# Kernel tuning notes

Hardware: AMD Instinct MI355X
Metric: run time of the kernel (lower is better)

The kernel has to match this reference:

```python
import math
import jax, jax.numpy as jnp
import numpy as np

TAU = 2.0
THR = 1.0
ALPHA = 10.0

T, B, IN_DIM, OUT_DIM = 64, 128, 2048, 2048


def setup_inputs() -> dict:
    key = jax.random.key(0)
    k1, k2, k3 = jax.random.split(key, 3)
    x_seq = jax.random.normal(k1, (T, B, IN_DIM), dtype=jnp.float32)
    # scale like nn.Linear default init so membrane potentials are O(1)
    W = jax.random.normal(k2, (OUT_DIM, IN_DIM), dtype=jnp.float32) / math.sqrt(IN_DIM)
    b = jax.random.normal(k3, (OUT_DIM,), dtype=jnp.float32) * 0.01
    return {"x_seq": x_seq, "W": W, "b": b}


def spike(x):
    # forward: hard threshold (surrogate gradient only matters in bwd)
    return (x > 0).astype(x.dtype)


def reference(x_seq, W, b):
    decay = math.exp(-1.0 / TAU)
    # hoist the linear layer out of the recurrence: one big GEMM
    cur_seq = jnp.einsum("tbi,oi->tbo", x_seq, W) + b  # (T, B, OUT_DIM)
    mem0 = jnp.zeros((x_seq.shape[1], W.shape[0]), dtype=x_seq.dtype)

    def step(mem, cur):
        mem = mem * decay + cur
        spk = spike(mem - THR)
        mem = mem - spk * THR
        return mem, spk

    _, spk_seq = jax.lax.scan(step, mem0, cur_seq)
    return spk_seq  # (T, B, OUT_DIM)
```

## Files before the change

### kernel.cpp

```cpp
#include <hip/hip_runtime.h>
#include <hip/hip_bf16.h>
#include <math.h>


typedef unsigned short u16;
typedef __attribute__((ext_vector_type(8))) short bf16x8;
typedef __attribute__((ext_vector_type(4))) float f32x4;

constexpr int T_STEPS = 64;
constexpr int BATCH   = 128;
constexpr int K_DIM   = 2048;
constexpr int N_DIM   = 2048;
constexpr int M_DIM   = T_STEPS * BATCH;
constexpr int NCHAIN  = BATCH * N_DIM;

constexpr float DECAY_F32 = (float)0.6065306597126334;
constexpr float BAND      = 5e-4f;

#define GLDS16(g, l) __builtin_amdgcn_global_load_lds(                       \
    (const __attribute__((address_space(1))) void*)(g),                      \
    (__attribute__((address_space(3))) void*)(l), 16, 0, 0)

__global__ void zero_counters(unsigned int* p) {
    if (threadIdx.x < 128) p[threadIdx.x] = 0u;
}

__global__ __launch_bounds__(256)
void split_bf16(const float* __restrict__ X, const float* __restrict__ W,
                u16* __restrict__ Ah, u16* __restrict__ Al,
                u16* __restrict__ Wh, u16* __restrict__ Wl) {
    constexpr int NA4 = (M_DIM * K_DIM) / 4;
    constexpr int NW4 = (N_DIM * K_DIM) / 4;
    const int i = blockIdx.x * 256 + threadIdx.x;
    const float* src; u16* dh; u16* dl; int base;
    if (i < NA4)            { src = X; dh = Ah; dl = Al; base = i; }
    else if (i < NA4 + NW4) { src = W; dh = Wh; dl = Wl; base = i - NA4; }
    else return;

    const float4 v = *(const float4*)(src + (size_t)base * 4);
    const float f[4] = {v.x, v.y, v.z, v.w};
    unsigned int hp[2], lp[2];
#pragma unroll
    for (int q = 0; q < 4; q += 2) {
        u16 hh[2], ll[2];
#pragma unroll
        for (int e = 0; e < 2; e++) {
            __hip_bfloat16 hb = __float2bfloat16(f[q + e]);
            const float hf = __bfloat162float(hb);
            __hip_bfloat16 lb = __float2bfloat16(f[q + e] - hf);
            hh[e] = *(u16*)&hb;
            ll[e] = *(u16*)&lb;
        }
        hp[q >> 1] = (unsigned int)hh[0] | ((unsigned int)hh[1] << 16);
        lp[q >> 1] = (unsigned int)ll[0] | ((unsigned int)ll[1] << 16);
    }
    *(uint2*)(dh + (size_t)base * 4) = make_uint2(hp[0], hp[1]);
    *(uint2*)(dl + (size_t)base * 4) = make_uint2(lp[0], lp[1]);
}

__global__ __launch_bounds__(512, 2)
void gemm_bf16x3p(const u16* __restrict__ Ah, const u16* __restrict__ Al,
                  const u16* __restrict__ Bh, const u16* __restrict__ Bl,
                  const float* __restrict__ bias, float* __restrict__ C) {
    extern __shared__ __align__(16) u16 smem[];
    u16* const sAh = smem;
    u16* const sAl = smem + 3 * 8192;
    u16* const sBh = smem + 6 * 8192;
    u16* const sBl = smem + 6 * 8192 + 3 * 4096;

    const int tid  = threadIdx.x;
    const int m0   = blockIdx.y * 256;
    const int n0   = blockIdx.x * 128;
    const int lane = tid & 63;
    const int wave = tid >> 6;
    const int wm   = wave >> 1;
    const int wn   = wave & 1;

    const int cA0 = tid, cA1 = tid + 512, cB0 = tid;
#define OFFA(c) ((size_t)(m0 + ((c) >> 6) * 16 + ((c) & 15)) * K_DIM + (((c) >> 4) & 3) * 8)
#define OFFB(c) ((size_t)(n0 + ((c) >> 6) * 16 + ((c) & 15)) * K_DIM + (((c) >> 4) & 3) * 8)
    const size_t a0 = OFFA(cA0), a1 = OFFA(cA1), b0 = OFFB(cB0);
#undef OFFA
#undef OFFB

    const int lA0 = wave * 512;
    const int lA1 = 4096 + wave * 512;
    const int lB0 = wave * 512;

    f32x4 acc[4][4];
#pragma unroll
    for (int i = 0; i < 4; i++)
#pragma unroll
        for (int j = 0; j < 4; j++) acc[i][j] = (f32x4){0.f, 0.f, 0.f, 0.f};

#define STAGE(s, kc) do {                                                    \
        const int kn_ = (kc) * 32;                                           \
        GLDS16(Ah + a0 + kn_, sAh + (s) * 8192 + lA0);                       \
        GLDS16(Ah + a1 + kn_, sAh + (s) * 8192 + lA1);                       \
        GLDS16(Al + a0 + kn_, sAl + (s) * 8192 + lA0);                       \
        GLDS16(Al + a1 + kn_, sAl + (s) * 8192 + lA1);                       \
        GLDS16(Bh + b0 + kn_, sBh + (s) * 4096 + lB0);                       \
        GLDS16(Bl + b0 + kn_, sBl + (s) * 4096 + lB0);                       \
    } while (0)

#define COMPUTE(rs) do {                                                     \
        bf16x8 fah[4], fal[4], fbh[4], fbl[4];                               \
        _Pragma("unroll")                                                    \
        for (int ti = 0; ti < 4; ti++) {                                     \
            const int ta = wm * 4 + ti;                                      \
            fah[ti] = *(const bf16x8*)&sAh[(rs) * 8192 + (ta * 64 + lane) * 8]; \
            fal[ti] = *(const bf16x8*)&sAl[(rs) * 8192 + (ta * 64 + lane) * 8]; \
        }                                                                    \
        _Pragma("unroll")                                                    \
        for (int tj = 0; tj < 4; tj++) {                                     \
            const int tb = wn * 4 + tj;                                      \
            fbh[tj] = *(const bf16x8*)&sBh[(rs) * 4096 + (tb * 64 + lane) * 8]; \
            fbl[tj] = *(const bf16x8*)&sBl[(rs) * 4096 + (tb * 64 + lane) * 8]; \
        }                                                                    \
        __builtin_amdgcn_s_setprio(1);                                       \
        _Pragma("unroll")                                                    \
        for (int ti = 0; ti < 4; ti++)                                       \
        _Pragma("unroll")                                                    \
        for (int tj = 0; tj < 4; tj++) {                                     \
            acc[ti][tj] = __builtin_amdgcn_mfma_f32_16x16x32_bf16(           \
                fah[ti], fbh[tj], acc[ti][tj], 0, 0, 0);                     \
            acc[ti][tj] = __builtin_amdgcn_mfma_f32_16x16x32_bf16(           \
                fah[ti], fbl[tj], acc[ti][tj], 0, 0, 0);                     \
            acc[ti][tj] = __builtin_amdgcn_mfma_f32_16x16x32_bf16(           \
                fal[ti], fbh[tj], acc[ti][tj], 0, 0, 0);                     \
        }                                                                    \
        __builtin_amdgcn_s_setprio(0);                                       \
    } while (0)

#define SYNC(vm) do {                                                        \
        asm volatile("s_waitcnt vmcnt(" #vm ")" ::: "memory");               \
        __builtin_amdgcn_sched_barrier(0);                                   \
        __builtin_amdgcn_s_barrier();                                        \
        __builtin_amdgcn_sched_barrier(0);                                   \
    } while (0)

    STAGE(0, 0);
    STAGE(1, 1);

    for (int kcb = 0; kcb < 63; kcb += 3) {
        SYNC(6);
        STAGE(2, kcb + 2);
        COMPUTE(0);
        SYNC(6);
        STAGE(0, kcb + 3);
        COMPUTE(1);
        SYNC(6);
        if (kcb + 4 < 64) STAGE(1, kcb + 4);
        COMPUTE(2);
    }
    SYNC(0);
    COMPUTE(0);

#undef SYNC
#undef COMPUTE
#undef STAGE

#pragma unroll
    for (int tj = 0; tj < 4; tj++) {
        const int n  = n0 + wn * 64 + tj * 16 + (lane & 15);
        const float bv = bias[n];
#pragma unroll
        for (int ti = 0; ti < 4; ti++) {
            const int mbase = m0 + wm * 64 + ti * 16 + (lane >> 4) * 4;
#pragma unroll
            for (int r = 0; r < 4; r++)
                C[(size_t)(mbase + r) * N_DIM + n] = acc[ti][tj][r] + bv;
        }
    }
}

__global__ __launch_bounds__(256)
void lif_scan_band(float* __restrict__ buf, unsigned int* __restrict__ counters,
                   unsigned int* __restrict__ worklist) {
    const int idx = blockIdx.x * 256 + threadIdx.x;
    float mem = 0.0f;
    bool flag = false;
#pragma unroll
    for (int t = 0; t < T_STEPS; t++) {
        const size_t off = (size_t)t * NCHAIN + idx;
        mem = __fadd_rn(__fmul_rn(mem, DECAY_F32), buf[off]);
        const float d = __fsub_rn(mem, 1.0f);
        const bool spk = d > 0.0f;
        if (fabsf(d) < BAND) flag = true;
        buf[off] = spk ? 1.0f : 0.0f;
        if (spk) mem = __fsub_rn(mem, 1.0f);
    }
    if (flag) {
        const int b = idx >> 11, o = idx & 2047;
        const unsigned int p = atomicAdd(&counters[b], 1u);
        worklist[b * 2048 + p] = (unsigned int)o;
    }
}

#define RG 16
#define RJ 4
#define BKR 64

__global__ __launch_bounds__(256)
void lif_repair2(const float* __restrict__ X, const float* __restrict__ W,
                 const float* __restrict__ bias,
                 const unsigned int* __restrict__ counters,
                 const unsigned int* __restrict__ worklist,
                 float* __restrict__ out) {
    __shared__ float sX[BKR][T_STEPS + 1];
    __shared__ float sW[RG][BKR + 1];
    __shared__ float scur[T_STEPS][RG + 1];
    __shared__ float sspk[T_STEPS][RG + 1];
    __shared__ int   so[RG];

    const int b = blockIdx.x / RJ;
    const int j = blockIdx.x % RJ;
    const unsigned int n_b = counters[b];
    if (n_b == 0) return;
    const int ngroups = (int)(n_b + RG - 1) / RG;

    const int tid = threadIdx.x;
    const int t   = tid & 63;
    const int oi  = tid >> 6;

    for (int g = j; g < ngroups; g += RJ) {
        if (tid < RG) {
            const int slot = g * RG + tid;
            so[tid] = (slot < (int)n_b) ? (int)worklist[b * 2048 + slot] : -1;
        }
        __syncthreads();

        float Csum[4] = {0.f, 0.f, 0.f, 0.f};
        float P[4]    = {0.f, 0.f, 0.f, 0.f};

        for (int c = 0; c < K_DIM / BKR; c++) {
            if (c > 0 && (c % 5) == 0) {
#pragma unroll
                for (int q = 0; q < 4; q++) {
                    Csum[q] = __fadd_rn(Csum[q], P[q]);
                    P[q] = 0.f;
                }
            }
            const int k0 = c * BKR;
            {
                const int ts = tid & 63;
                const int kq = (tid >> 6) * 16;
                const float* src = &X[(size_t)(ts * BATCH + b) * K_DIM + k0 + kq];
#pragma unroll
                for (int q = 0; q < 4; q++) {
                    const float4 v = *(const float4*)(src + q * 4);
                    sX[kq + q * 4 + 0][ts] = v.x;
                    sX[kq + q * 4 + 1][ts] = v.y;
                    sX[kq + q * 4 + 2][ts] = v.z;
                    sX[kq + q * 4 + 3][ts] = v.w;
                }
            }
            {
                const int wo  = tid >> 4;
                const int wkq = (tid & 15) * 4;
                const int o   = so[wo];
                float4 v = {0.f, 0.f, 0.f, 0.f};
                if (o >= 0) v = *(const float4*)&W[(size_t)o * K_DIM + k0 + wkq];
                sW[wo][wkq + 0] = v.x; sW[wo][wkq + 1] = v.y;
                sW[wo][wkq + 2] = v.z; sW[wo][wkq + 3] = v.w;
            }
            __syncthreads();
#pragma unroll 8
            for (int k = 0; k < BKR; k++) {
                const float xv = sX[k][t];
#pragma unroll
                for (int q = 0; q < 4; q++)
                    P[q] = fmaf(xv, sW[oi * 4 + q][k], P[q]);
            }
            __syncthreads();
        }
#pragma unroll
        for (int q = 0; q < 4; q++) {
            Csum[q] = __fadd_rn(Csum[q], P[q]);
            const int o = so[oi * 4 + q];
            scur[t][oi * 4 + q] = (o >= 0) ? __fadd_rn(Csum[q], bias[o]) : 0.f;
        }
        __syncthreads();
        if (tid < RG && so[tid] >= 0) {
            float mem = 0.0f;
            for (int tt = 0; tt < T_STEPS; tt++) {
                mem = __fadd_rn(__fmul_rn(mem, DECAY_F32), scur[tt][tid]);
                const float d = __fsub_rn(mem, 1.0f);
                const bool spk = d > 0.0f;
                sspk[tt][tid] = spk ? 1.0f : 0.0f;
                if (spk) mem = __fsub_rn(mem, 1.0f);
            }
        }
        __syncthreads();
#pragma unroll
        for (int q = 0; q < 4; q++) {
            const int o = so[oi * 4 + q];
            if (o >= 0)
                out[(size_t)t * NCHAIN + (size_t)b * N_DIM + o] = sspk[t][oi * 4 + q];
        }
        __syncthreads();
    }
}

__global__ __launch_bounds__(256)
void lif_openblas_q320(const float* __restrict__ X, const float* __restrict__ W,
                       const float* __restrict__ bias, float* __restrict__ out) {
    __shared__ float As[16][T_STEPS + 4];
    __shared__ float Ws[16][64 + 4];
    __shared__ float curbuf[T_STEPS][64 + 1];
    const int tid = threadIdx.x;
    const int o0 = blockIdx.x * 64, b0 = blockIdx.y;
    const int tm = (tid & 15) * 4, tn = (tid >> 4) * 4;
    float Csum[4][4], Pacc[4][4];
#pragma unroll
    for (int i = 0; i < 4; i++)
#pragma unroll
        for (int j = 0; j < 4; j++) { Csum[i][j] = 0.f; Pacc[i][j] = 0.f; }
    for (int c = 0; c < K_DIM / 16; c++) {
        if (c > 0 && (c % 20) == 0) {
#pragma unroll
            for (int i = 0; i < 4; i++)
#pragma unroll
                for (int j = 0; j < 4; j++) {
                    Csum[i][j] = __fadd_rn(Csum[i][j], Pacc[i][j]);
                    Pacc[i][j] = 0.f;
                }
        }
        const int k0 = c * 16;
        {
            const int t = tid >> 2, kq = (tid & 3) * 4;
            const float4 av = *(const float4*)&X[(size_t)(t * BATCH + b0) * K_DIM + k0 + kq];
            As[kq + 0][t] = av.x; As[kq + 1][t] = av.y;
            As[kq + 2][t] = av.z; As[kq + 3][t] = av.w;
            const float4 wv = *(const float4*)&W[(size_t)(o0 + t) * K_DIM + k0 + kq];
            Ws[kq + 0][t] = wv.x; Ws[kq + 1][t] = wv.y;
            Ws[kq + 2][t] = wv.z; Ws[kq + 3][t] = wv.w;
        }
        __syncthreads();
#pragma unroll
        for (int k = 0; k < 16; k++) {
            float a[4], w[4];
#pragma unroll
            for (int i = 0; i < 4; i++) a[i] = As[k][tm + i];
#pragma unroll
            for (int j = 0; j < 4; j++) w[j] = Ws[k][tn + j];
#pragma unroll
            for (int i = 0; i < 4; i++)
#pragma unroll
                for (int j = 0; j < 4; j++) Pacc[i][j] = fmaf(a[i], w[j], Pacc[i][j]);
        }
        __syncthreads();
    }
#pragma unroll
    for (int i = 0; i < 4; i++)
#pragma unroll
        for (int j = 0; j < 4; j++)
            curbuf[tm + i][tn + j] =
                __fadd_rn(__fadd_rn(Csum[i][j], Pacc[i][j]), bias[o0 + tn + j]);
    __syncthreads();
    if (tid < 64) {
        float mem = 0.0f;
#pragma unroll
        for (int t = 0; t < T_STEPS; t++) {
            mem = __fadd_rn(__fmul_rn(mem, DECAY_F32), curbuf[t][tid]);
            const float d = __fsub_rn(mem, 1.0f);
            const bool spk = d > 0.0f;
            out[(size_t)t * NCHAIN + (size_t)b0 * N_DIM + o0 + tid] = spk ? 1.0f : 0.0f;
            if (spk) mem = __fsub_rn(mem, 1.0f);
        }
    }
}

extern "C" void kernel_launch(void* const* d_in, const int* in_sizes, int n_in,
                              void* d_out, int out_size, void* d_ws, size_t ws_size,
                              hipStream_t stream) {
    const float* x = nullptr; const float* W = nullptr; const float* bias = nullptr;
    for (int i = 0; i < n_in; i++) {
        if      (in_sizes[i] == M_DIM * K_DIM) x    = (const float*)d_in[i];
        else if (in_sizes[i] == N_DIM * K_DIM) W    = (const float*)d_in[i];
        else if (in_sizes[i] == N_DIM)         bias = (const float*)d_in[i];
    }
    if (!x)    x    = (const float*)d_in[0];
    if (!W)    W    = (const float*)d_in[1];
    if (!bias) bias = (const float*)d_in[2];
    float* out = (float*)d_out;

    const size_t off_cnt = 0;
    const size_t off_wl  = 512;
    const size_t off_Ah  = off_wl + (size_t)128 * 2048 * 4;
    const size_t szA     = (size_t)M_DIM * K_DIM * 2;
    const size_t szW     = (size_t)N_DIM * K_DIM * 2;
    const size_t off_Al  = off_Ah + szA;
    const size_t off_Wh  = off_Al + szA;
    const size_t off_Wl  = off_Wh + szW;
    const size_t need    = off_Wl + szW;

    if (ws_size < need) {
        dim3 grid(N_DIM / 64, BATCH);
        lif_openblas_q320<<<grid, 256, 0, stream>>>(x, W, bias, out);
        return;
    }

    char* ws = (char*)d_ws;
    unsigned int* counters = (unsigned int*)(ws + off_cnt);
    unsigned int* worklist = (unsigned int*)(ws + off_wl);
    u16* Ah = (u16*)(ws + off_Ah);
    u16* Al = (u16*)(ws + off_Al);
    u16* Wh = (u16*)(ws + off_Wh);
    u16* Wl = (u16*)(ws + off_Wl);

    zero_counters<<<1, 128, 0, stream>>>(counters);
    split_bf16<<<(M_DIM * K_DIM / 4 + N_DIM * K_DIM / 4) / 256, 256, 0, stream>>>(
        x, W, Ah, Al, Wh, Wl);
    dim3 ggrid(N_DIM / 128, M_DIM / 256);
    gemm_bf16x3p<<<ggrid, 512, 147456, stream>>>(Ah, Al, Wh, Wl, bias, out);
    lif_scan_band<<<NCHAIN / 256, 256, 0, stream>>>(out, counters, worklist);
    lif_repair2<<<128 * RJ, 256, 0, stream>>>(x, W, bias, counters, worklist, out);
}
```

Before: 481.6 us.

## Double-buffer GEMM register fragments and fold counter zeroing into split kernel

The GEMM main loop now keeps two register fragment sets, loading the next K-chunk from LDS while MFMAs run on the current one. It also prefetches three LDS stages up front and rotates stage indices, with the wait extended to include lgkmcnt. The counter-zeroing launch is merged into the split kernel, removing one kernel launch, and the repair kernel's X tile load is remapped so consecutive threads read contiguous K segments for better coalescing. The extra fragment registers raise VGPR pressure, which may hurt occupancy at 512 threads with 2 blocks per CU.

Result: no change. 472.2 us (-1.9%).

```diff
diff --git a/kernel.cpp b/kernel.cpp
--- a/kernel.cpp
+++ b/kernel.cpp
@@ -21,14 +21,13 @@
     (const __attribute__((address_space(1))) void*)(g),                      \
     (__attribute__((address_space(3))) void*)(l), 16, 0, 0)
 
-__global__ void zero_counters(unsigned int* p) {
-    if (threadIdx.x < 128) p[threadIdx.x] = 0u;
-}
-
 __global__ __launch_bounds__(256)
 void split_bf16(const float* __restrict__ X, const float* __restrict__ W,
                 u16* __restrict__ Ah, u16* __restrict__ Al,
-                u16* __restrict__ Wh, u16* __restrict__ Wl) {
+                u16* __restrict__ Wh, u16* __restrict__ Wl,
+                unsigned int* __restrict__ counters) {
+    if (blockIdx.x == 0 && threadIdx.x < 128) counters[threadIdx.x] = 0u;
+
     constexpr int NA4 = (M_DIM * K_DIM) / 4;
     constexpr int NW4 = (N_DIM * K_DIM) / 4;
     const int i = blockIdx.x * 256 + threadIdx.x;
@@ -59,7 +58,7 @@
 }
 
 __global__ __launch_bounds__(512, 2)
-void gemm_bf16x3p(const u16* __restrict__ Ah, const u16* __restrict__ Al,
+void gemm_bf16x3q(const u16* __restrict__ Ah, const u16* __restrict__ Al,
                   const u16* __restrict__ Bh, const u16* __restrict__ Bl,
                   const float* __restrict__ bias, float* __restrict__ C) {
     extern __shared__ __align__(16) u16 smem[];
@@ -93,47 +92,54 @@
 #pragma unroll
         for (int j = 0; j < 4; j++) acc[i][j] = (f32x4){0.f, 0.f, 0.f, 0.f};
 
+    bf16x8 fahA[4], falA[4], fbhA[4], fblA[4];
+    bf16x8 fahB[4], falB[4], fbhB[4], fblB[4];
+
 #define STAGE(s, kc) do {                                                    \
         const int kn_ = (kc) * 32;                                           \
-        GLDS16(Ah + a0 + kn_, sAh + (s) * 8192 + lA0);                       \
-        GLDS16(Ah + a1 + kn_, sAh + (s) * 8192 + lA1);                       \
-        GLDS16(Al + a0 + kn_, sAl + (s) * 8192 + lA0);                       \
-        GLDS16(Al + a1 + kn_, sAl + (s) * 8192 + lA1);                       \
-        GLDS16(Bh + b0 + kn_, sBh + (s) * 4096 + lB0);                       \
-        GLDS16(Bl + b0 + kn_, sBl + (s) * 4096 + lB0);                       \
+        const int sA_ = (s) * 8192, sB_ = (s) * 4096;                        \
+        GLDS16(Ah + a0 + kn_, sAh + sA_ + lA0);                              \
+        GLDS16(Ah + a1 + kn_, sAh + sA_ + lA1);                              \
+        GLDS16(Al + a0 + kn_, sAl + sA_ + lA0);                              \
+        GLDS16(Al + a1 + kn_, sAl + sA_ + lA1);                              \
+        GLDS16(Bh + b0 + kn_, sBh + sB_ + lB0);                              \
+        GLDS16(Bl + b0 + kn_, sBl + sB_ + lB0);                              \
     } while (0)
 
-#define COMPUTE(rs) do {                                                     \
-        bf16x8 fah[4], fal[4], fbh[4], fbl[4];                               \
+#define LOADF(SET, s) do {                                                   \
+        const int sA_ = (s) * 8192, sB_ = (s) * 4096;                        \
         _Pragma("unroll")                                                    \
         for (int ti = 0; ti < 4; ti++) {                                     \
             const int ta = wm * 4 + ti;                                      \
-            fah[ti] = *(const bf16x8*)&sAh[(rs) * 8192 + (ta * 64 + lane) * 8]; \
-            fal[ti] = *(const bf16x8*)&sAl[(rs) * 8192 + (ta * 64 + lane) * 8]; \
+            fah##SET[ti] = *(const bf16x8*)&sAh[sA_ + (ta * 64 + lane) * 8]; \
+            fal##SET[ti] = *(const bf16x8*)&sAl[sA_ + (ta * 64 + lane) * 8]; \
         }                                                                    \
         _Pragma("unroll")                                                    \
         for (int tj = 0; tj < 4; tj++) {                                     \
             const int tb = wn * 4 + tj;                                      \
-            fbh[tj] = *(const bf16x8*)&sBh[(rs) * 4096 + (tb * 64 + lane) * 8]; \
-            fbl[tj] = *(const bf16x8*)&sBl[(rs) * 4096 + (tb * 64 + lane) * 8]; \
+            fbh##SET[tj] = *(const bf16x8*)&sBh[sB_ + (tb * 64 + lane) * 8]; \
+            fbl##SET[tj] = *(const bf16x8*)&sBl[sB_ + (tb * 64 + lane) * 8]; \
         }                                                                    \
+    } while (0)
+
+#define COMPUTE(SET) do {                                                    \
         __builtin_amdgcn_s_setprio(1);                                       \
         _Pragma("unroll")                                                    \
         for (int ti = 0; ti < 4; ti++)                                       \
         _Pragma("unroll")                                                    \
         for (int tj = 0; tj < 4; tj++) {                                     \
             acc[ti][tj] = __builtin_amdgcn_mfma_f32_16x16x32_bf16(           \
-                fah[ti], fbh[tj], acc[ti][tj], 0, 0, 0);                     \
+                fah##SET[ti], fbh##SET[tj], acc[ti][tj], 0, 0, 0);           \
             acc[ti][tj] = __builtin_amdgcn_mfma_f32_16x16x32_bf16(           \
-                fah[ti], fbl[tj], acc[ti][tj], 0, 0, 0);                     \
+                fah##SET[ti], fbl##SET[tj], acc[ti][tj], 0, 0, 0);           \
             acc[ti][tj] = __builtin_amdgcn_mfma_f32_16x16x32_bf16(           \
-                fal[ti], fbh[tj], acc[ti][tj], 0, 0, 0);                     \
+                fal##SET[ti], fbh##SET[tj], acc[ti][tj], 0, 0, 0);           \
         }                                                                    \
         __builtin_amdgcn_s_setprio(0);                                       \
     } while (0)
 
-#define SYNC(vm) do {                                                        \
-        asm volatile("s_waitcnt vmcnt(" #vm ")" ::: "memory");               \
+#define WAITSYNC(vm) do {                                                    \
+        asm volatile("s_waitcnt vmcnt(" #vm ") lgkmcnt(0)" ::: "memory");    \
         __builtin_amdgcn_sched_barrier(0);                                   \
         __builtin_amdgcn_s_barrier();                                        \
         __builtin_amdgcn_sched_barrier(0);                                   \
@@ -141,23 +147,33 @@
 
     STAGE(0, 0);
     STAGE(1, 1);
-
-    for (int kcb = 0; kcb < 63; kcb += 3) {
-        SYNC(6);
-        STAGE(2, kcb + 2);
-        COMPUTE(0);
-        SYNC(6);
-        STAGE(0, kcb + 3);
-        COMPUTE(1);
-        SYNC(6);
-        if (kcb + 4 < 64) STAGE(1, kcb + 4);
-        COMPUTE(2);
-    }
-    SYNC(0);
-    COMPUTE(0);
-
-#undef SYNC
+    STAGE(2, 2);
+    WAITSYNC(12);
+    LOADF(A, 0);
+
+    int s1 = 1, sW = 0;
+    for (int kc = 0; kc < 62; kc += 2) {
+        WAITSYNC(6);
+        LOADF(B, s1);
+        if (kc + 3 < 64) STAGE(sW, kc + 3);
+        COMPUTE(A);
+        s1 = (s1 == 2) ? 0 : s1 + 1;
+        sW = (sW == 2) ? 0 : sW + 1;
+        WAITSYNC(6);
+        LOADF(A, s1);
+        if (kc + 4 < 64) STAGE(sW, kc + 4);
+        COMPUTE(B);
+        s1 = (s1 == 2) ? 0 : s1 + 1;
+        sW = (sW == 2) ? 0 : sW + 1;
+    }
+    WAITSYNC(0);
+    LOADF(B, s1);
+    COMPUTE(A);
+    COMPUTE(B);
+
+#undef WAITSYNC
 #undef COMPUTE
+#undef LOADF
 #undef STAGE
 
 #pragma unroll
@@ -243,8 +259,8 @@
             }
             const int k0 = c * BKR;
             {
-                const int ts = tid & 63;
-                const int kq = (tid >> 6) * 16;
+                const int ts = tid >> 2;
+                const int kq = (tid & 3) * 16;
                 const float* src = &X[(size_t)(ts * BATCH + b) * K_DIM + k0 + kq];
 #pragma unroll
                 for (int q = 0; q < 4; q++) {
@@ -409,11 +425,10 @@
     u16* Wh = (u16*)(ws + off_Wh);
     u16* Wl = (u16*)(ws + off_Wl);
 
-    zero_counters<<<1, 128, 0, stream>>>(counters);
     split_bf16<<<(M_DIM * K_DIM / 4 + N_DIM * K_DIM / 4) / 256, 256, 0, stream>>>(
-        x, W, Ah, Al, Wh, Wl);
+        x, W, Ah, Al, Wh, Wl, counters);
     dim3 ggrid(N_DIM / 128, M_DIM / 256);
-    gemm_bf16x3p<<<ggrid, 512, 147456, stream>>>(Ah, Al, Wh, Wl, bias, out);
+    gemm_bf16x3q<<<ggrid, 512, 147456, stream>>>(Ah, Al, Wh, Wl, bias, out);
     lif_scan_band<<<NCHAIN / 256, 256, 0, stream>>>(out, counters, worklist);
     lif_repair2<<<128 * RJ, 256, 0, stream>>>(x, W, bias, counters, worklist, out);
 }
```
